# Kernel optimization log

Hardware: AMD Instinct MI355X
Metric: run time of the kernel (lower is better)

Reference implementation:

```python
import jax, jax.numpy as jnp
import numpy as np

RADIUS = 2.0   # sample_radius_m
KP = 4         # sample_keypoints
LEVELS = 2     # feature_levels


def _keypoints():
    return jnp.array([[0.0, 0.0, 0.0], [RADIUS, 0.0, 0.0],
                      [0.0, RADIUS, 0.0], [-RADIUS, 0.0, 0.0]], dtype=jnp.float32)


def _bilinear_sample(fm, x, y):
    # fm: [B,V,C,H,W]; x,y: [B,V,N] pixel coords. Bilinear, zeros padding,
    # matching F.grid_sample(align_corners=True, padding_mode='zeros').
    B, V, C, H, W = fm.shape
    N = x.shape[-1]
    x0 = jnp.floor(x); y0 = jnp.floor(y)
    x1 = x0 + 1.0;     y1 = y0 + 1.0
    wx1 = x - x0; wx0 = 1.0 - wx1
    wy1 = y - y0; wy0 = 1.0 - wy1
    fm_flat = fm.reshape(B, V, C, H * W)

    def gather(xi, yi):
        inb = ((xi >= 0) & (xi <= W - 1) & (yi >= 0) & (yi <= H - 1)).astype(fm.dtype)
        xc = jnp.clip(xi, 0, W - 1).astype(jnp.int32)
        yc = jnp.clip(yi, 0, H - 1).astype(jnp.int32)
        idx = (yc * W + xc)[:, :, None, :]                      # [B,V,1,N]
        vals = jnp.take_along_axis(fm_flat, jnp.broadcast_to(idx, (B, V, C, N)), axis=3)
        return vals * inb[:, :, None, :]                        # [B,V,C,N]

    out = (gather(x0, y0) * (wx0 * wy0)[:, :, None, :]
           + gather(x1, y0) * (wx1 * wy0)[:, :, None, :]
           + gather(x0, y1) * (wx0 * wy1)[:, :, None, :]
           + gather(x1, y1) * (wx1 * wy1)[:, :, None, :])
    return out  # [B,V,C,N]


def _level_sample(fm, refs, intrinsics, extrinsics):
    # fm: [B,V,C,H,W]; refs: [B,N,3] with N = Q*KP
    B, V, C, H, W = fm.shape
    N = refs.shape[1]
    Q = N // KP
    homo = jnp.concatenate([refs, jnp.ones(refs.shape[:-1] + (1,), refs.dtype)], axis=-1)
    cam = jnp.einsum('bvij,bnj->bvni', extrinsics, homo)[..., :3]   # world -> camera
    uvw = jnp.einsum('bvij,bvnj->bvni', intrinsics, cam)            # pinhole projection
    z = uvw[..., 2]                                                 # [B,V,N]
    uv = uvw[..., :2] / jnp.maximum(z, 1e-5)[..., None]
    valid = (z > 0.0).astype(fm.dtype)                              # [B,V,N]
    # normalize_grid (align_corners=True) then back to pixel coords
    gx = 2.0 * uv[..., 0] / (W - 1) - 1.0
    gy = 2.0 * uv[..., 1] / (H - 1) - 1.0
    x = (gx + 1.0) * (W - 1) / 2.0
    y = (gy + 1.0) * (H - 1) / 2.0
    vals = _bilinear_sample(fm, x, y) * valid[:, :, None, :]        # [B,V,C,N]
    vals = vals.reshape(B, V, C, Q, KP)
    valid = valid.reshape(B, V, Q, KP)
    num = vals.sum(axis=(1, 4))                                     # [B,C,Q] sum over views+keypoints
    cnt = jnp.maximum(valid.sum(axis=(1, 3)), 1.0)                  # [B,Q], clamp after view sum
    return (num / cnt[:, None, :]).transpose(0, 2, 1)               # [B,Q,C]


def setup_inputs() -> dict:
    key = jax.random.key(0)
    ks = jax.random.split(key, 6)
    B, V, C, Q = 4, 6, 256, 2048
    feat0 = jax.random.normal(ks[0], (B, V, C, 64, 176), dtype=jnp.float32)
    feat1 = jax.random.normal(ks[1], (B, V, C, 32, 88), dtype=jnp.float32)
    # 3D references: x,y in [-20,20], z (depth-ish) in [1,60]
    u = jax.random.uniform(ks[2], (B, Q, 3), dtype=jnp.float32)
    refs_xyz = jnp.stack([u[..., 0] * 40.0 - 20.0,
                          u[..., 1] * 40.0 - 20.0,
                          u[..., 2] * 59.0 + 1.0], axis=-1)
    # pinhole intrinsics in feature-map pixel units
    fx, fy, cx, cy = 60.0, 60.0, 88.0, 32.0
    K = jnp.array([[fx, 0.0, cx], [0.0, fy, cy], [0.0, 0.0, 1.0]], dtype=jnp.float32)
    intrinsics = jnp.broadcast_to(K, (B, V, 3, 3)) \
        + 0.01 * jax.random.normal(ks[3], (B, V, 3, 3), dtype=jnp.float32)
    # extrinsics: identity rotation + small random translation, world pts face +z
    E = jnp.eye(4, dtype=jnp.float32)
    t = 0.5 * jax.random.normal(ks[4], (B, V, 3), dtype=jnp.float32)
    extrinsics = jnp.broadcast_to(E, (B, V, 4, 4)).at[:, :, :3, 3].set(t)
    return {"feat0": feat0, "feat1": feat1, "refs_xyz": refs_xyz,
            "intrinsics": intrinsics, "extrinsics": extrinsics}


def reference(feat0, feat1, refs_xyz, intrinsics, extrinsics):
    B, Q = refs_xyz.shape[:2]
    kp = _keypoints()
    refs = (refs_xyz[:, :, None, :] + kp[None, None, :, :]).reshape(B, Q * KP, 3)
    out = _level_sample(feat0, refs, intrinsics, extrinsics)
    out = out + _level_sample(feat1, refs, intrinsics, extrinsics)
    return out / float(LEVELS)
```

## Files before the change

kernel.cpp:

```cpp
#include <hip/hip_runtime.h>
#include <math.h>

#define B_ 4
#define V_ 6
#define C_ 256
#define Q_ 2048
#define KP_ 4
#define H0_ 64
#define W0_ 176
#define H1_ 32
#define W1_ 88
#define RADIUS_ 2.0f

#define HW0_ (H0_ * W0_)
#define HW1_ (H1_ * W1_)
#define NQ_  (B_ * Q_)

#define F0_ELEMS ((size_t)B_ * V_ * C_ * HW0_)
#define F1_ELEMS ((size_t)B_ * V_ * C_ * HW1_)

#define T0_TILES_ (HW0_ / 64 * B_ * V_)
#define T1_TILES_ (HW1_ / 64 * B_ * V_)

typedef float f4 __attribute__((ext_vector_type(4)));
typedef unsigned short us8 __attribute__((ext_vector_type(8)));

__device__ __forceinline__ unsigned short f2bf(float f) {
  const unsigned int x = __float_as_uint(f);
  return (unsigned short)((x + 0x7fffu + ((x >> 16) & 1u)) >> 16);
}
__device__ __forceinline__ float bf2f(unsigned short u) {
  return __uint_as_float((unsigned int)u << 16);
}

__global__ __launch_bounds__(256) void proj_kernel(
    const float* __restrict__ refs,
    const float* __restrict__ intr,
    const float* __restrict__ extr,
    float* __restrict__ xy,
    unsigned int* __restrict__ masks, float* __restrict__ invs) {
  const int idx = blockIdx.x * 256 + threadIdx.x;
  if (idx >= NQ_) return;
  const int b = idx >> 11;
  const float rx = refs[(size_t)idx * 3 + 0];
  const float ry = refs[(size_t)idx * 3 + 1];
  const float rz = refs[(size_t)idx * 3 + 2];
  unsigned int mask = 0;
  const size_t base = (size_t)idx * 48;
  for (int v = 0; v < V_; ++v) {
    const float* E = extr + ((size_t)b * V_ + v) * 16;
    const float* K = intr + ((size_t)b * V_ + v) * 9;
    for (int kp = 0; kp < KP_; ++kp) {
      const float kx = (kp == 1) ? RADIUS_ : ((kp == 3) ? -RADIUS_ : 0.f);
      const float ky = (kp == 2) ? RADIUS_ : 0.f;
      const float px = rx + kx, py = ry + ky, pz = rz;
      const float cx = E[0] * px + E[1] * py + E[2]  * pz + E[3];
      const float cy = E[4] * px + E[5] * py + E[6]  * pz + E[7];
      const float cz = E[8] * px + E[9] * py + E[10] * pz + E[11];
      const float uu = K[0] * cx + K[1] * cy + K[2] * cz;
      const float vv = K[3] * cx + K[4] * cy + K[5] * cz;
      const float ww = K[6] * cx + K[7] * cy + K[8] * cz;
      const float zc = fmaxf(ww, 1e-5f);
      const int s = v * KP_ + kp;
      xy[base + 2 * s]     = uu / zc;
      xy[base + 2 * s + 1] = vv / zc;
      if (ww > 0.f) mask |= (1u << s);
    }
  }
  masks[idx] = mask;
  invs[idx] = 0.5f / fmaxf((float)__popc(mask), 1.0f);
}

__global__ __launch_bounds__(256) void transpose_bf16(
    const float* __restrict__ f0, const float* __restrict__ f1,
    unsigned short* __restrict__ f0t, unsigned short* __restrict__ f1t) {
  __shared__ float tile[64][69];
  int bx = blockIdx.x;
  const float* src; unsigned short* dst; int HW, bv, ptile;
  if (bx < T0_TILES_) {
    src = f0; dst = f0t; HW = HW0_;
    bv = bx / (HW0_ / 64); ptile = bx % (HW0_ / 64);
  } else {
    bx -= T0_TILES_;
    src = f1; dst = f1t; HW = HW1_;
    bv = bx / (HW1_ / 64); ptile = bx % (HW1_ / 64);
  }
  const int p0 = ptile * 64;
  const int ct0 = blockIdx.y * 64;
  const size_t sbase = (size_t)bv * C_ * HW;
  const size_t dbase = (size_t)bv * HW * C_;
  const int tid = threadIdx.x;

  {
    const int px4 = (tid & 15) * 4;
    const int crow = tid >> 4;
    for (int j = 0; j < 64; j += 16) {
      const f4 v = __builtin_nontemporal_load(
          reinterpret_cast<const f4*>(
              src + sbase + (size_t)(ct0 + crow + j) * HW + p0 + px4));
      tile[crow + j][px4 + 0] = v.x;
      tile[crow + j][px4 + 1] = v.y;
      tile[crow + j][px4 + 2] = v.z;
      tile[crow + j][px4 + 3] = v.w;
    }
  }
  __syncthreads();
  {
    const int cx8 = (tid & 7) * 8;
    const int prow = tid >> 3;
    for (int j = 0; j < 64; j += 32) {
      us8 o;
      #pragma unroll
      for (int k = 0; k < 8; ++k) o[k] = f2bf(tile[cx8 + k][prow + j]);
      *reinterpret_cast<us8*>(
          dst + dbase + (size_t)(p0 + prow + j) * C_ + ct0 + cx8) = o;
    }
  }
}

__global__ __launch_bounds__(256) void sampler_bf16(
    const unsigned short* __restrict__ f0t,
    const unsigned short* __restrict__ f1t,
    const float* __restrict__ xy,
    const unsigned int* __restrict__ masks, const float* __restrict__ invs,
    float* __restrict__ out) {
  const int tid = threadIdx.x;
  const int wave = __builtin_amdgcn_readfirstlane(tid >> 6);
  const int lane = tid & 63;
  const int half = lane >> 5;
  const int cidx = lane & 31;
  const int idx = blockIdx.x * 4 + wave;
  const int b = idx >> 11;

  const unsigned int mask = masks[idx];
  const float inv = invs[idx];
  const float* pxy = xy + (size_t)idx * 48;
  const int ce = cidx * 8;

  const unsigned short* F0 = f0t + (size_t)b * V_ * HW0_ * C_ + ce;
  const unsigned short* F1 = f1t + (size_t)b * V_ * HW1_ * C_ + ce;

  float acc[8] = {0.f, 0.f, 0.f, 0.f, 0.f, 0.f, 0.f, 0.f};

  #pragma unroll
  for (int s = 0; s < 24; ++s) {
    const bool valid = (mask >> s) & 1u;
    float x = pxy[2 * s], y = pxy[2 * s + 1];
    if (!valid) { x = 0.f; y = 0.f; }
    const float fvalid = valid ? 1.f : 0.f;
    const float x0f = floorf(x), y0f = floorf(y);
    const float wx1 = x - x0f, wy1 = y - y0f;
    const float wx0 = 1.f - wx1, wy0 = 1.f - wy1;
    const int v = s >> 2;

    {
      const float Wm1 = (float)(W0_ - 1), Hm1 = (float)(H0_ - 1);
      const float xhf = half ? (x0f + 1.f) : x0f;
      const float bx = (xhf >= 0.f && xhf <= Wm1) ? 1.f : 0.f;
      const float by0 = (y0f >= 0.f && y0f <= Hm1) ? 1.f : 0.f;
      const float by1 = (y0f + 1.f >= 0.f && y0f + 1.f <= Hm1) ? 1.f : 0.f;
      const float wxh = (half ? wx1 : wx0) * bx * fvalid;
      const int xh  = (int)fminf(fmaxf(xhf, 0.f), Wm1);
      const int yi0 = (int)fminf(fmaxf(y0f, 0.f), Hm1);
      const int yi1 = (int)fminf(fmaxf(y0f + 1.f, 0.f), Hm1);
      const float w0 = wxh * wy0 * by0;
      const float w1 = wxh * wy1 * by1;
      const int pix0 = (w0 != 0.f) ? (yi0 * W0_ + xh) : 0;
      const int pix1 = (w1 != 0.f) ? (yi1 * W0_ + xh) : 0;
      const unsigned short* Fv = F0 + (size_t)v * HW0_ * C_;
      const us8 u0 = *reinterpret_cast<const us8*>(Fv + (size_t)pix0 * C_);
      const us8 u1 = *reinterpret_cast<const us8*>(Fv + (size_t)pix1 * C_);
      #pragma unroll
      for (int k = 0; k < 8; ++k) {
        acc[k] = fmaf(w0, bf2f(u0[k]), acc[k]);
        acc[k] = fmaf(w1, bf2f(u1[k]), acc[k]);
      }
    }

    {
      const float Wm1 = (float)(W1_ - 1), Hm1 = (float)(H1_ - 1);
      const float x1f = x0f + 1.f, y1f = y0f + 1.f;
      const bool bx0 = (x0f >= 0.f) && (x0f <= Wm1);
      const bool bx1 = (x1f >= 0.f) && (x1f <= Wm1);
      const bool by0 = (y0f >= 0.f) && (y0f <= Hm1);
      const bool by1 = (y1f >= 0.f) && (y1f <= Hm1);
      if (((bx0 || bx1) && (by0 || by1)) && valid) {
        const int xi0 = (int)fminf(fmaxf(x0f, 0.f), Wm1);
        const int xi1 = (int)fminf(fmaxf(x1f, 0.f), Wm1);
        const int xh = half ? xi1 : xi0;
        const float wxh = half ? (bx1 ? wx1 : 0.f) : (bx0 ? wx0 : 0.f);
        const int yi0 = (int)fminf(fmaxf(y0f, 0.f), Hm1);
        const int yi1 = (int)fminf(fmaxf(y1f, 0.f), Hm1);
        const float w0 = wxh * wy0 * (by0 ? 1.f : 0.f);
        const float w1 = wxh * wy1 * (by1 ? 1.f : 0.f);
        const int pix0 = (w0 != 0.f) ? (yi0 * W1_ + xh) : 0;
        const int pix1 = (w1 != 0.f) ? (yi1 * W1_ + xh) : 0;
        const unsigned short* Fv = F1 + (size_t)v * HW1_ * C_;
        const us8 u0 = *reinterpret_cast<const us8*>(Fv + (size_t)pix0 * C_);
        const us8 u1 = *reinterpret_cast<const us8*>(Fv + (size_t)pix1 * C_);
        #pragma unroll
        for (int k = 0; k < 8; ++k) {
          acc[k] = fmaf(w0, bf2f(u0[k]), acc[k]);
          acc[k] = fmaf(w1, bf2f(u1[k]), acc[k]);
        }
      }
    }
  }

  #pragma unroll
  for (int k = 0; k < 8; ++k) acc[k] += __shfl_xor(acc[k], 32);

  f4 o;
  const int ko = half * 4;
  o.x = acc[ko + 0] * inv;
  o.y = acc[ko + 1] * inv;
  o.z = acc[ko + 2] * inv;
  o.w = acc[ko + 3] * inv;
  __builtin_nontemporal_store(
      o, reinterpret_cast<f4*>(out + (size_t)idx * C_ + ce + ko));
}

__device__ __forceinline__ float bilinear_scalar(
    const float* __restrict__ fm, const int W, const int H,
    const float x, const float y) {
  const float x0f = floorf(x), y0f = floorf(y);
  const float wx1 = x - x0f, wy1 = y - y0f;
  const float wx0 = 1.f - wx1, wy0 = 1.f - wy1;
  const float x1f = x0f + 1.f, y1f = y0f + 1.f;
  const float Wm1 = (float)(W - 1), Hm1 = (float)(H - 1);
  const bool bx0 = (x0f >= 0.f) && (x0f <= Wm1);
  const bool bx1 = (x1f >= 0.f) && (x1f <= Wm1);
  const bool by0 = (y0f >= 0.f) && (y0f <= Hm1);
  const bool by1 = (y1f >= 0.f) && (y1f <= Hm1);
  if (!((bx0 || bx1) && (by0 || by1))) return 0.f;
  const int xi0 = (int)fminf(fmaxf(x0f, 0.f), Wm1);
  const int xi1 = (int)fminf(fmaxf(x1f, 0.f), Wm1);
  const int yi0 = (int)fminf(fmaxf(y0f, 0.f), Hm1);
  const int yi1 = (int)fminf(fmaxf(y1f, 0.f), Hm1);
  float r = 0.f;
  if (bx0 && by0) r = fmaf(wx0 * wy0, fm[yi0 * W + xi0], r);
  if (bx1 && by0) r = fmaf(wx1 * wy0, fm[yi0 * W + xi1], r);
  if (bx0 && by1) r = fmaf(wx0 * wy1, fm[yi1 * W + xi0], r);
  if (bx1 && by1) r = fmaf(wx1 * wy1, fm[yi1 * W + xi1], r);
  return r;
}

__global__ __launch_bounds__(256) void sampler_direct(
    const float* __restrict__ f0, const float* __restrict__ f1,
    const float* __restrict__ refs, const float* __restrict__ intr,
    const float* __restrict__ extr, float* __restrict__ out) {
  __shared__ float sx[24], sy[24], scnt;
  __shared__ unsigned int smask;
  const int tid = threadIdx.x;
  const int b = blockIdx.y, q = blockIdx.x;
  bool zvalid = false;
  if (tid < 24) {
    const int v = tid >> 2, kp = tid & 3;
    const float kx = (kp == 1) ? RADIUS_ : ((kp == 3) ? -RADIUS_ : 0.f);
    const float ky = (kp == 2) ? RADIUS_ : 0.f;
    const float rx = refs[((size_t)b * Q_ + q) * 3 + 0];
    const float ry = refs[((size_t)b * Q_ + q) * 3 + 1];
    const float rz = refs[((size_t)b * Q_ + q) * 3 + 2];
    const float px = rx + kx, py = ry + ky, pz = rz;
    const float* E = extr + ((size_t)b * V_ + v) * 16;
    const float cx = E[0] * px + E[1] * py + E[2]  * pz + E[3];
    const float cy = E[4] * px + E[5] * py + E[6]  * pz + E[7];
    const float cz = E[8] * px + E[9] * py + E[10] * pz + E[11];
    const float* K = intr + ((size_t)b * V_ + v) * 9;
    const float uu = K[0] * cx + K[1] * cy + K[2] * cz;
    const float vv = K[3] * cx + K[4] * cy + K[5] * cz;
    const float ww = K[6] * cx + K[7] * cy + K[8] * cz;
    const float zc = fmaxf(ww, 1e-5f);
    sx[tid] = uu / zc;
    sy[tid] = vv / zc;
    zvalid = (ww > 0.f);
  }
  const unsigned long long m = __ballot(zvalid);
  if (tid == 0) {
    const unsigned int mm = (unsigned int)(m & 0xFFFFFFULL);
    smask = mm;
    scnt = fmaxf((float)__popc(mm), 1.0f);
  }
  __syncthreads();
  const unsigned int mask = smask;
  const float cnt = scnt;
  const int c = tid;
  float a0 = 0.f, a1 = 0.f;
  for (int s = 0; s < 24; ++s) {
    if (!((mask >> s) & 1u)) continue;
    const float x = sx[s], y = sy[s];
    const int v = s >> 2;
    const size_t bv = (size_t)b * V_ + v;
    a0 += bilinear_scalar(f0 + (bv * C_ + c) * (size_t)HW0_, W0_, H0_, x, y);
    a1 += bilinear_scalar(f1 + (bv * C_ + c) * (size_t)HW1_, W1_, H1_, x, y);
  }
  out[((size_t)b * Q_ + q) * C_ + c] = (a0 + a1) * 0.5f / cnt;
}

extern "C" void kernel_launch(void* const* d_in, const int* in_sizes, int n_in,
                              void* d_out, int out_size, void* d_ws, size_t ws_size,
                              hipStream_t stream) {
  const float* feat0 = (const float*)d_in[0];
  const float* feat1 = (const float*)d_in[1];
  const float* refs  = (const float*)d_in[2];
  const float* intr  = (const float*)d_in[3];
  const float* extr  = (const float*)d_in[4];
  float* out = (float*)d_out;

  const size_t need = F0_ELEMS * 2 + F1_ELEMS * 2
                    + ((size_t)NQ_ * 48 + 2 * NQ_) * 4;

  if (ws_size >= need) {
    unsigned short* f0t = (unsigned short*)d_ws;
    unsigned short* f1t = f0t + F0_ELEMS;
    float* xy = (float*)(f1t + F1_ELEMS);
    unsigned int* masks = (unsigned int*)(xy + (size_t)NQ_ * 48);
    float* invs = (float*)(masks + NQ_);

    proj_kernel<<<NQ_ / 256, 256, 0, stream>>>(refs, intr, extr, xy, masks, invs);
    transpose_bf16<<<dim3(T0_TILES_ + T1_TILES_, C_ / 64), 256, 0, stream>>>(
        feat0, feat1, f0t, f1t);
    sampler_bf16<<<dim3(NQ_ / 4), 256, 0, stream>>>(
        f0t, f1t, xy, masks, invs, out);
  } else {
    sampler_direct<<<dim3(Q_, B_), 256, 0, stream>>>(
        feat0, feat1, refs, intr, extr, out);
  }
}
```

Baseline: 151.4 us.

## Bucket queries by projected image tile to improve gather cache locality

Adds a counting sort of queries by the 16x16 image tile that their first keypoint projects to in view 0, per batch. The buckets are built with atomics in the projection kernel, then a serial prefix scan and a placement pass, and the sampler reads its query index through the resulting map, with blocks interleaved across the 8 XCDs. The intent is that spatially nearby queries run together and reuse feature-map lines in L2. In exchange it adds three small kernel launches and a single-threaded scan, and the bucketing only looks at view 0.

```diff
diff --git a/kernel.cpp b/kernel.cpp
--- a/kernel.cpp
+++ b/kernel.cpp
@@ -22,6 +22,9 @@
 #define T0_TILES_ (HW0_ / 64 * B_ * V_)
 #define T1_TILES_ (HW1_ / 64 * B_ * V_)
 
+#define NBK_ 44
+#define NBKT_ (NBK_ * B_)
+
 typedef float f4 __attribute__((ext_vector_type(4)));
 typedef unsigned short us8 __attribute__((ext_vector_type(8)));
 
@@ -31,6 +34,10 @@
 }
 __device__ __forceinline__ float bf2f(unsigned short u) {
   return __uint_as_float((unsigned int)u << 16);
+}
+
+__global__ __launch_bounds__(256) void zero_kernel(unsigned int* __restrict__ cnt) {
+  if (threadIdx.x < NBKT_) cnt[threadIdx.x] = 0;
 }
 
 __global__ __launch_bounds__(256) void proj_kernel(
@@ -38,7 +45,8 @@
     const float* __restrict__ intr,
     const float* __restrict__ extr,
     float* __restrict__ xy,
-    unsigned int* __restrict__ masks, float* __restrict__ invs) {
+    unsigned int* __restrict__ masks, float* __restrict__ invs,
+    int* __restrict__ key, unsigned int* __restrict__ cnt) {
   const int idx = blockIdx.x * 256 + threadIdx.x;
   if (idx >= NQ_) return;
   const int b = idx >> 11;
@@ -47,6 +55,7 @@
   const float rz = refs[(size_t)idx * 3 + 2];
   unsigned int mask = 0;
   const size_t base = (size_t)idx * 48;
+  float kx0 = 0.f, ky0 = 0.f;
   for (int v = 0; v < V_; ++v) {
     const float* E = extr + ((size_t)b * V_ + v) * 16;
     const float* K = intr + ((size_t)b * V_ + v) * 9;
@@ -62,13 +71,40 @@
       const float ww = K[6] * cx + K[7] * cy + K[8] * cz;
       const float zc = fmaxf(ww, 1e-5f);
       const int s = v * KP_ + kp;
-      xy[base + 2 * s]     = uu / zc;
-      xy[base + 2 * s + 1] = vv / zc;
+      const float xs = uu / zc, ys = vv / zc;
+      xy[base + 2 * s]     = xs;
+      xy[base + 2 * s + 1] = ys;
+      if (s == 0) { kx0 = xs; ky0 = ys; }
       if (ww > 0.f) mask |= (1u << s);
     }
   }
   masks[idx] = mask;
   invs[idx] = 0.5f / fmaxf((float)__popc(mask), 1.0f);
+  const int bx = (int)fminf(fmaxf(kx0, 0.f), (float)(W0_ - 1)) >> 4;
+  const int by = (int)fminf(fmaxf(ky0, 0.f), (float)(H0_ - 1)) >> 4;
+  const int k = b * NBK_ + by * 11 + bx;
+  key[idx] = k;
+  atomicAdd(&cnt[k], 1u);
+}
+
+__global__ void prefix_kernel(unsigned int* __restrict__ cnt) {
+  if (threadIdx.x == 0 && blockIdx.x == 0) {
+    unsigned int run = 0;
+    for (int i = 0; i < NBKT_; ++i) {
+      const unsigned int c = cnt[i];
+      cnt[i] = run;
+      run += c;
+    }
+  }
+}
+
+__global__ __launch_bounds__(256) void place_kernel(
+    const int* __restrict__ key, unsigned int* __restrict__ cursor,
+    int* __restrict__ qmap) {
+  const int idx = blockIdx.x * 256 + threadIdx.x;
+  if (idx >= NQ_) return;
+  const unsigned int pos = atomicAdd(&cursor[key[idx]], 1u);
+  qmap[pos] = idx;
 }
 
 __global__ __launch_bounds__(256) void transpose_bf16(
@@ -123,13 +159,15 @@
     const unsigned short* __restrict__ f1t,
     const float* __restrict__ xy,
     const unsigned int* __restrict__ masks, const float* __restrict__ invs,
+    const int* __restrict__ qmap,
     float* __restrict__ out) {
   const int tid = threadIdx.x;
   const int wave = __builtin_amdgcn_readfirstlane(tid >> 6);
   const int lane = tid & 63;
   const int half = lane >> 5;
   const int cidx = lane & 31;
-  const int idx = blockIdx.x * 4 + wave;
+  const int lblk = ((int)blockIdx.x & 7) * 256 + ((int)blockIdx.x >> 3);
+  const int idx = qmap[lblk * 4 + wave];
   const int b = idx >> 11;
 
   const unsigned int mask = masks[idx];
@@ -308,7 +346,8 @@
   float* out = (float*)d_out;
 
   const size_t need = F0_ELEMS * 2 + F1_ELEMS * 2
-                    + ((size_t)NQ_ * 48 + 2 * NQ_) * 4;
+                    + ((size_t)NQ_ * 48 + 2 * NQ_) * 4
+                    + (2 * (size_t)NQ_ + NBKT_) * 4;
 
   if (ws_size >= need) {
     unsigned short* f0t = (unsigned short*)d_ws;
@@ -316,12 +355,19 @@
     float* xy = (float*)(f1t + F1_ELEMS);
     unsigned int* masks = (unsigned int*)(xy + (size_t)NQ_ * 48);
     float* invs = (float*)(masks + NQ_);
-
-    proj_kernel<<<NQ_ / 256, 256, 0, stream>>>(refs, intr, extr, xy, masks, invs);
+    int* key = (int*)(invs + NQ_);
+    int* qmap = key + NQ_;
+    unsigned int* cnt = (unsigned int*)(qmap + NQ_);
+
+    zero_kernel<<<1, 256, 0, stream>>>(cnt);
+    proj_kernel<<<NQ_ / 256, 256, 0, stream>>>(
+        refs, intr, extr, xy, masks, invs, key, cnt);
+    prefix_kernel<<<1, 64, 0, stream>>>(cnt);
+    place_kernel<<<NQ_ / 256, 256, 0, stream>>>(key, cnt, qmap);
     transpose_bf16<<<dim3(T0_TILES_ + T1_TILES_, C_ / 64), 256, 0, stream>>>(
         feat0, feat1, f0t, f1t);
     sampler_bf16<<<dim3(NQ_ / 4), 256, 0, stream>>>(
-        f0t, f1t, xy, masks, invs, out);
+        f0t, f1t, xy, masks, invs, qmap, out);
   } else {
     sampler_direct<<<dim3(Q_, B_), 256, 0, stream>>>(
         feat0, feat1, refs, intr, extr, out);
```

Measured after the change: 157.2 us. 1.04x slower.
